# Optimization experiments

Hardware: AMD Instinct MI355X
Metric: run time of the kernel (lower is better)

## Reference

```python
import jax, jax.numpy as jnp
import numpy as np

WINDOW = (2, 8, 8)  # (T, H, W); N = 128
NUM_HEADS = 6
DIM = 192


def _relative_position_index(ws):
    """NxN int index into the relative-position-bias table (faithful port)."""
    d, h, w = np.meshgrid(np.arange(ws[0]), np.arange(ws[1]), np.arange(ws[2]), indexing='ij')
    coords = np.stack([d, h, w]).reshape(3, -1)            # (3, N)
    rel = coords[:, :, None] - coords[:, None, :]          # (3, N, N)
    rel = rel.transpose(1, 2, 0).astype(np.int64)          # (N, N, 3)
    rel[:, :, 0] += ws[0] - 1
    rel[:, :, 1] += ws[1] - 1
    rel[:, :, 2] += ws[2] - 1
    rel[:, :, 0] *= (2 * ws[1] - 1) * (2 * ws[2] - 1)
    rel[:, :, 1] *= 2 * ws[2] - 1
    return rel.sum(-1)                                     # (N, N)


def setup_inputs() -> dict:
    key = jax.random.key(0)
    k1, k2, k3, k4, k5, k6 = jax.random.split(key, 6)
    N = WINDOW[0] * WINDOW[1] * WINDOW[2]                  # 128
    B_ = 1024                                              # num_windows * batch
    nW = 64
    table_len = (2 * WINDOW[0] - 1) * (2 * WINDOW[1] - 1) * (2 * WINDOW[2] - 1)  # 675
    x = jax.random.normal(k1, (B_, N, DIM), dtype=jnp.float32)
    mask = jax.random.normal(k2, (nW, N, N), dtype=jnp.float32)  # additive attn mask
    qkv_w = jax.random.normal(k3, (3 * DIM, DIM), dtype=jnp.float32) * 0.02
    proj_w = jax.random.normal(k4, (DIM, DIM), dtype=jnp.float32) * 0.02
    proj_b = jax.random.normal(k5, (DIM,), dtype=jnp.float32) * 0.02
    rpb_table = jax.random.normal(k6, (table_len, NUM_HEADS), dtype=jnp.float32) * 0.02
    rel_index = jnp.asarray(_relative_position_index(WINDOW), dtype=jnp.int32)
    return {"x": x, "mask": mask, "qkv_w": qkv_w, "proj_w": proj_w,
            "proj_b": proj_b, "rpb_table": rpb_table, "rel_index": rel_index}


def reference(x, mask, qkv_w, proj_w, proj_b, rpb_table, rel_index):
    B_, N, C = x.shape
    H = NUM_HEADS
    hd = C // H
    scale = hd ** (-0.5)
    # qkv projection (no bias, qkv_bias=False)
    qkv = (x @ qkv_w.T).reshape(B_, N, 3, H, hd)
    q, k, v = qkv[:, :, 0], qkv[:, :, 1], qkv[:, :, 2]      # (B_, N, H, hd)
    # windowed attention scores
    attn = jnp.einsum('bnhd,bmhd->bhnm', q * scale, k)      # (B_, H, N, N)
    # gathered relative-position bias: (N, N, H) -> (H, N, N)
    bias = rpb_table[rel_index.reshape(-1)].reshape(N, N, H).transpose(2, 0, 1)
    attn = attn + bias[None]
    # shift-window mask: (nW, N, N) broadcast over batch groups and heads
    nW = mask.shape[0]
    attn = attn.reshape(B_ // nW, nW, H, N, N) + mask[None, :, None]
    attn = attn.reshape(B_, H, N, N)
    attn = jax.nn.softmax(attn, axis=-1)
    out = jnp.einsum('bhnm,bmhd->bnhd', attn, v).reshape(B_, N, C)
    return out @ proj_w.T + proj_b
```

## Files before the change

### kernel.cpp

```cpp
#include <hip/hip_runtime.h>
#include <hip/hip_bf16.h>


typedef float f32x4 __attribute__((ext_vector_type(4)));
typedef short short8 __attribute__((ext_vector_type(8)));
typedef short short4e __attribute__((ext_vector_type(4)));

#define SCALE 0.17677669529663687f
#define LOG2E 1.4426950408889634f
#define QSC (SCALE * LOG2E)

#define GLOAD16(src, dst)                                                      \
  __builtin_amdgcn_global_load_lds(                                            \
      (const __attribute__((address_space(1))) unsigned int*)(const void*)(src),\
      (__attribute__((address_space(3))) unsigned int*)(void*)(dst), 16, 0, 0)

static __device__ __forceinline__ short f2bf(float f) {
  __hip_bfloat16 h = __float2bfloat16(f);
  return __builtin_bit_cast(short, h);
}
static __device__ __forceinline__ f32x4 mfma16(short8 a, short8 b, f32x4 c) {
  return __builtin_amdgcn_mfma_f32_16x16x32_bf16(a, b, c, 0, 0, 0);
}

__global__ __launch_bounds__(256) void prep_w(const float* __restrict__ qkvw,
                                              const float* __restrict__ projw,
                                              short* __restrict__ wbf,
                                              short* __restrict__ pwbf) {
  int t = blockIdx.x * 256 + threadIdx.x;
  const int NQ = 27648;
  float4 f; short* dst;
  if (t < NQ) {
    f = ((const float4*)qkvw)[t];
    int row = (t * 4) / 192, c4 = (t * 4) % 192;
    dst = wbf + row * 192 + (c4 ^ ((row & 7) << 3));
  } else {
    f = ((const float4*)projw)[t - NQ];
    dst = pwbf + (t - NQ) * 4;
  }
  short4e o; o[0] = f2bf(f.x); o[1] = f2bf(f.y); o[2] = f2bf(f.z); o[3] = f2bf(f.w);
  *(short4e*)dst = o;
}

__global__ __launch_bounds__(256) void prep_bm(const int* __restrict__ rel,
                                               const float* __restrict__ table,
                                               const float* __restrict__ mask,
                                               float* __restrict__ bmF) {
  int blk = blockIdx.x;
  int h = blk >> 6, w = blk & 63;
  int tid = threadIdx.x, lane = tid & 63, wave = tid >> 6;
  int lr = lane & 15, r4 = (lane >> 4) * 4;
  const float* mk = mask + (size_t)w * 16384;
  float* dst = bmF + (size_t)blk * 16384;
#pragma unroll
  for (int L = 0; L < 16; ++L) {
    int rf = L >> 3, rg = (L >> 1) & 3, cp = L & 1;
    int row = wave * 32 + rf * 16 + r4 + rg;
    float4 v;
#pragma unroll
    for (int e = 0; e < 4; ++e) {
      int col = (cp * 4 + e) * 16 + lr;
      float bias = table[rel[row * 128 + col] * 6 + h];
      ((float*)&v)[e] = (bias + mk[row * 128 + col]) * LOG2E;
    }
    ((float4*)dst)[L * 256 + tid] = v;
  }
}

__global__ __launch_bounds__(256, 4) void qkv_kernel(const float* __restrict__ x,
                                                     const short* __restrict__ wbf,
                                                     short* __restrict__ qb,
                                                     short* __restrict__ kb,
                                                     short* __restrict__ vb) {
  __shared__ short wt[2][6144];
  char* wtb = (char*)wt;
  const int b = blockIdx.x, tid = threadIdx.x;
  const int wave = tid >> 6, lane = tid & 63;
  const int lr = lane & 15, g = lane >> 4, g8 = g * 8, r4 = g * 4;
  const int rowbase = wave * 32;
  const int xorkey = (lr & 7) << 4;
  const int wl = wave * 1024 + lane * 16;
  const int wu = wave * 1024;

  short8 xa[2][6];
  {
    const float* xr = x + (size_t)b * 24576 + (size_t)(rowbase + lr) * 192;
#pragma unroll
    for (int tf = 0; tf < 2; ++tf)
#pragma unroll
      for (int ks = 0; ks < 6; ++ks) {
        const float* p = xr + tf * 16 * 192 + ks * 32 + g8;
        float4 f0 = *(const float4*)p;
        float4 f1 = *(const float4*)(p + 4);
        short8 v8;
        v8[0] = f2bf(f0.x); v8[1] = f2bf(f0.y); v8[2] = f2bf(f0.z); v8[3] = f2bf(f0.w);
        v8[4] = f2bf(f1.x); v8[5] = f2bf(f1.y); v8[6] = f2bf(f1.z); v8[7] = f2bf(f1.w);
        xa[tf][ks] = v8;
      }
  }
  {
    const char* wsrc = (const char*)wbf;
#pragma unroll
    for (int i = 0; i < 3; ++i)
      GLOAD16(wsrc + i * 4096 + wl, wtb + i * 4096 + wu);
  }
  __syncthreads();

  for (int ch = 0; ch < 12; ++ch) {
    {
      const char* wsrc = (const char*)wbf + (ch + 1) * 12288;
      char* wdst = wtb + ((ch + 1) & 1) * 12288;
#pragma unroll
      for (int i = 0; i < 3; ++i)
        GLOAD16(wsrc + i * 4096 + wl, wdst + i * 4096 + wu);
    }
    const char* wb = wtb + (ch & 1) * 12288;
    f32x4 acc[2][2];
    acc[0][0] = acc[0][1] = acc[1][0] = acc[1][1] = f32x4{0.f, 0.f, 0.f, 0.f};
    __builtin_amdgcn_s_setprio(1);
#pragma unroll
    for (int ks = 0; ks < 6; ++ks) {
      int cx = (ks * 64 + g * 16) ^ xorkey;
      short8 w0 = *(const short8*)(wb + lr * 384 + cx);
      short8 w1 = *(const short8*)(wb + (16 + lr) * 384 + cx);
      acc[0][0] = mfma16(w0, xa[0][ks], acc[0][0]);
      acc[0][1] = mfma16(w0, xa[1][ks], acc[0][1]);
      acc[1][0] = mfma16(w1, xa[0][ks], acc[1][0]);
      acc[1][1] = mfma16(w1, xa[1][ks], acc[1][1]);
    }
    __builtin_amdgcn_s_setprio(0);
    bool isq = (ch < 6);
    short* dst = isq ? qb : kb;
    int h = isq ? ch : ch - 6;
    float sc = isq ? QSC : 1.0f;
    size_t base = ((size_t)b * 6 + h) * 4096;
#pragma unroll
    for (int cf = 0; cf < 2; ++cf)
#pragma unroll
      for (int tf = 0; tf < 2; ++tf) {
        int tok = rowbase + tf * 16 + lr;
        int col = cf * 16 + r4;
        int idx = isq ? col : (col ^ (((tok >> 1) & 3) << 3));
        short4e s4;
        s4[0] = f2bf(acc[cf][tf][0] * sc);
        s4[1] = f2bf(acc[cf][tf][1] * sc);
        s4[2] = f2bf(acc[cf][tf][2] * sc);
        s4[3] = f2bf(acc[cf][tf][3] * sc);
        *(short4e*)&dst[base + (size_t)tok * 32 + idx] = s4;
      }
    __syncthreads();
  }
  for (int ch = 12; ch < 18; ++ch) {
    if (ch < 17) {
      const char* wsrc = (const char*)wbf + (ch + 1) * 12288;
      char* wdst = wtb + ((ch + 1) & 1) * 12288;
#pragma unroll
      for (int i = 0; i < 3; ++i)
        GLOAD16(wsrc + i * 4096 + wl, wdst + i * 4096 + wu);
    }
    const char* wb = wtb + (ch & 1) * 12288;
    f32x4 acc[2][2];
    acc[0][0] = acc[0][1] = acc[1][0] = acc[1][1] = f32x4{0.f, 0.f, 0.f, 0.f};
    __builtin_amdgcn_s_setprio(1);
#pragma unroll
    for (int ks = 0; ks < 6; ++ks) {
      int cx = (ks * 64 + g * 16) ^ xorkey;
      short8 w0 = *(const short8*)(wb + lr * 384 + cx);
      short8 w1 = *(const short8*)(wb + (16 + lr) * 384 + cx);
      acc[0][0] = mfma16(xa[0][ks], w0, acc[0][0]);
      acc[0][1] = mfma16(xa[0][ks], w1, acc[0][1]);
      acc[1][0] = mfma16(xa[1][ks], w0, acc[1][0]);
      acc[1][1] = mfma16(xa[1][ks], w1, acc[1][1]);
    }
    __builtin_amdgcn_s_setprio(0);
    int h = ch - 12;
    size_t base = ((size_t)b * 6 + h) * 4096;
#pragma unroll
    for (int tf = 0; tf < 2; ++tf)
#pragma unroll
      for (int cf = 0; cf < 2; ++cf) {
        int d = cf * 16 + lr;
        int rowpos = rowbase + tf * 16 + r4;
        short4e s4;
        s4[0] = f2bf(acc[tf][cf][0]);
        s4[1] = f2bf(acc[tf][cf][1]);
        s4[2] = f2bf(acc[tf][cf][2]);
        s4[3] = f2bf(acc[tf][cf][3]);
        *(short4e*)&vb[base + (size_t)d * 128 + (rowpos ^ ((d & 15) << 3))] = s4;
      }
    if (ch < 17) __syncthreads();
  }
}

__global__ __launch_bounds__(256, 4) void attn_kernel(const short* __restrict__ qb,
                                                      const short* __restrict__ kb,
                                                      const short* __restrict__ vb,
                                                      const float* __restrict__ bmF,
                                                      char* __restrict__ outc) {
  __shared__ char sbuf[16384];
  __shared__ short p_lds[8192];
  const int bh = blockIdx.x, b = bh / 6, h = bh - b * 6;
  const short* qt = qb + (size_t)bh * 4096;
  const char* kc = (const char*)(kb + (size_t)bh * 4096);
  const char* vc = (const char*)(vb + (size_t)bh * 4096);
  const float4* bm4 = (const float4*)(bmF + ((size_t)h * 64 + (b & 63)) * 16384);
  short* outSlot = (short*)(outc + (size_t)b * 98304 + 49152);
  const int tid = threadIdx.x, wave = tid >> 6, lane = tid & 63;
  const int lr = lane & 15, g = lane >> 4, r4 = g * 4;
  const int rowbase = wave * 32;
  const int wl = wave * 1024 + lane * 16;
  const int wu = wave * 1024;

  GLOAD16(kc + wl,        sbuf + wu);
  GLOAD16(kc + 4096 + wl, sbuf + 4096 + wu);
  GLOAD16(vc + wl,        sbuf + 8192 + wu);
  GLOAD16(vc + 4096 + wl, sbuf + 12288 + wu);
  short8 qaH[2];
  qaH[0] = *(const short8*)&qt[(rowbase + lr) * 32 + g * 8];
  qaH[1] = *(const short8*)&qt[(rowbase + 16 + lr) * 32 + g * 8];
  __syncthreads();

  const char* ksb = sbuf;
  const char* vs = sbuf + 8192;
  char* pw = (char*)p_lds + wave * 4096;
  const int kkey = ((lr >> 1) & 3) << 4;

#pragma unroll
  for (int rf = 0; rf < 2; ++rf) {
    float4 bmv[8];
#pragma unroll
    for (int i = 0; i < 8; ++i) bmv[i] = bm4[(rf * 8 + i) * 256 + tid];
    short8 qa = qaH[rf];
    f32x4 s[8];
    __builtin_amdgcn_s_setprio(1);
#pragma unroll
    for (int cf = 0; cf < 8; ++cf) {
      int krow = cf * 16 + lr;
      short8 kf = *(const short8*)(ksb + krow * 64 + ((g * 16) ^ kkey));
      f32x4 z = {0.f, 0.f, 0.f, 0.f};
      s[cf] = mfma16(qa, kf, z);
    }
    __builtin_amdgcn_s_setprio(0);
    float inv_[4];
#pragma unroll
    for (int rg = 0; rg < 4; ++rg) {
      float4 bb0 = bmv[rg * 2];
      float4 bb1 = bmv[rg * 2 + 1];
      float p0 = exp2f(s[0][rg] + bb0.x);
      float p1 = exp2f(s[1][rg] + bb0.y);
      float p2 = exp2f(s[2][rg] + bb0.z);
      float p3 = exp2f(s[3][rg] + bb0.w);
      float p4 = exp2f(s[4][rg] + bb1.x);
      float p5 = exp2f(s[5][rg] + bb1.y);
      float p6 = exp2f(s[6][rg] + bb1.z);
      float p7 = exp2f(s[7][rg] + bb1.w);
      float sum = ((p0 + p1) + (p2 + p3)) + ((p4 + p5) + (p6 + p7));
#pragma unroll
      for (int o = 1; o < 16; o <<= 1) sum += __shfl_xor(sum, o);
      inv_[rg] = 1.0f / sum;
      int rr = r4 + rg;
      int base = rr * 256 + (lr << 1);
      int swz = rr << 4;
      *(short*)(pw + ((base + 0 * 32) ^ swz)) = f2bf(p0);
      *(short*)(pw + ((base + 1 * 32) ^ swz)) = f2bf(p1);
      *(short*)(pw + ((base + 2 * 32) ^ swz)) = f2bf(p2);
      *(short*)(pw + ((base + 3 * 32) ^ swz)) = f2bf(p3);
      *(short*)(pw + ((base + 4 * 32) ^ swz)) = f2bf(p4);
      *(short*)(pw + ((base + 5 * 32) ^ swz)) = f2bf(p5);
      *(short*)(pw + ((base + 6 * 32) ^ swz)) = f2bf(p6);
      *(short*)(pw + ((base + 7 * 32) ^ swz)) = f2bf(p7);
    }
    f32x4 o0 = {0.f, 0.f, 0.f, 0.f}, o1 = {0.f, 0.f, 0.f, 0.f};
#pragma unroll
    for (int kst = 0; kst < 4; ++kst) {
      short8 pa = *(const short8*)(pw + ((lr * 256 + kst * 64 + g * 16) ^ (lr << 4)));
      short8 vb0 = *(const short8*)(vs + ((lr * 256 + kst * 64 + g * 16) ^ ((lr & 15) << 4)));
      short8 vb1 = *(const short8*)(vs + (((16 + lr) * 256 + kst * 64 + g * 16) ^ (((16 + lr) & 15) << 4)));
      __builtin_amdgcn_s_setprio(1);
      o0 = mfma16(pa, vb0, o0);
      o1 = mfma16(pa, vb1, o1);
      __builtin_amdgcn_s_setprio(0);
    }
#pragma unroll
    for (int rg = 0; rg < 4; ++rg) {
      int tok = rowbase + rf * 16 + r4 + rg;
      float iv = inv_[rg];
      outSlot[(size_t)tok * 192 + h * 32 + lr] = f2bf(o0[rg] * iv);
      outSlot[(size_t)tok * 192 + h * 32 + 16 + lr] = f2bf(o1[rg] * iv);
    }
  }
}

__global__ __launch_bounds__(256, 2) void proj_kernel(const short* __restrict__ pwbf,
                                                      const float* __restrict__ pb,
                                                      float* __restrict__ out) {
  __shared__ short at[24576];
  __shared__ short wt[2][6144];
  const int b = blockIdx.x, tid = threadIdx.x;
  const int wave = tid >> 6, lane = tid & 63;
  const int lr = lane & 15, g = lane >> 4;
  const int g16 = g * 16, r4 = g * 4;
  const int rowbase = wave * 32;
  const int xorkey = (lr & 7) << 4;
  char* atb = (char*)at;
  char* wtb = (char*)wt;

  int wsoff[3], wdoff[3];
#pragma unroll
  for (int i = 0; i < 3; ++i) {
    int idx8 = i * 256 + tid;
    int r = idx8 / 24, c = idx8 - r * 24;
    wsoff[i] = idx8 * 8;
    wdoff[i] = r * 384 + ((c * 16) ^ ((r & 7) << 4));
  }
  short8 wreg[3];
#pragma unroll
  for (int i = 0; i < 3; ++i) wreg[i] = *(const short8*)(pwbf + wsoff[i]);

  const short8* ar = (const short8*)((const char*)out + (size_t)b * 98304 + 49152);
#pragma unroll
  for (int i = 0; i < 12; ++i) {
    int idx8 = i * 256 + tid;
    int r = idx8 / 24, c = idx8 - r * 24;
    short8 v = ar[idx8];
    *(short8*)(atb + r * 384 + ((c * 16) ^ ((r & 7) << 4))) = v;
  }
#pragma unroll
  for (int i = 0; i < 3; ++i) *(short8*)(wtb + wdoff[i]) = wreg[i];
  __syncthreads();

  const int rA0 = (rowbase + lr) * 384, rA1 = rA0 + 16 * 384;
  const int wB0 = lr * 384, wB1 = wB0 + 16 * 384;

  for (int ch = 0; ch < 6; ++ch) {
    if (ch < 5) {
#pragma unroll
      for (int i = 0; i < 3; ++i)
        wreg[i] = *(const short8*)(pwbf + (ch + 1) * 6144 + wsoff[i]);
    }
    const char* wbuf = wtb + (ch & 1) * 12288;
    f32x4 acc[2][2];
    acc[0][0] = acc[0][1] = acc[1][0] = acc[1][1] = f32x4{0.f, 0.f, 0.f, 0.f};
#pragma unroll
    for (int ks = 0; ks < 6; ++ks) {
      int cx = (ks * 64 + g16) ^ xorkey;
      short8 xa0 = *(const short8*)(atb + rA0 + cx);
      short8 xa1 = *(const short8*)(atb + rA1 + cx);
      short8 wf0 = *(const short8*)(wbuf + wB0 + cx);
      short8 wf1 = *(const short8*)(wbuf + wB1 + cx);
      acc[0][0] = mfma16(xa0, wf0, acc[0][0]);
      acc[0][1] = mfma16(xa0, wf1, acc[0][1]);
      acc[1][0] = mfma16(xa1, wf0, acc[1][0]);
      acc[1][1] = mfma16(xa1, wf1, acc[1][1]);
    }
#pragma unroll
    for (int cf = 0; cf < 2; ++cf) {
      int j = ch * 32 + cf * 16 + lr;
      float bj = pb[j];
#pragma unroll
      for (int rf = 0; rf < 2; ++rf)
#pragma unroll
        for (int rg = 0; rg < 4; ++rg) {
          int tok = rowbase + rf * 16 + r4 + rg;
          out[((size_t)b * 128 + tok) * 192 + j] = acc[rf][cf][rg] + bj;
        }
    }
    if (ch < 5) {
#pragma unroll
      for (int i = 0; i < 3; ++i)
        *(short8*)(wtb + ((ch + 1) & 1) * 12288 + wdoff[i]) = wreg[i];
      __syncthreads();
    }
  }
}

extern "C" void kernel_launch(void* const* d_in, const int* in_sizes, int n_in,
                              void* d_out, int out_size, void* d_ws, size_t ws_size,
                              hipStream_t stream) {
  const float* x      = (const float*)d_in[0];
  const float* mask   = (const float*)d_in[1];
  const float* qkv_w  = (const float*)d_in[2];
  const float* proj_w = (const float*)d_in[3];
  const float* proj_b = (const float*)d_in[4];
  const float* table  = (const float*)d_in[5];
  const int*   rel    = (const int*)d_in[6];
  char* ws = (char*)d_ws;
  size_t o = 0;
  float* bmF  = (float*)(ws + o); o += 25165824;
  short* wbf  = (short*)(ws + o); o += 221184;
  short* pwbf = (short*)(ws + o); o += 73728;
  short* qbp  = (short*)(ws + o); o += 50331648;
  short* kbp  = (short*)(ws + o); o += 50331648;
  short* vbp  = (short*)(ws + o); o += 50331648;
  float* out = (float*)d_out;

  prep_w<<<144, 256, 0, stream>>>(qkv_w, proj_w, wbf, pwbf);
  prep_bm<<<384, 256, 0, stream>>>(rel, table, mask, bmF);
  qkv_kernel<<<1024, 256, 0, stream>>>(x, wbf, qbp, kbp, vbp);
  attn_kernel<<<6144, 256, 0, stream>>>(qbp, kbp, vbp, bmF, (char*)d_out);
  proj_kernel<<<1024, 256, 0, stream>>>(pwbf, proj_b, (float*)d_out);
}
```

Measured before the change: 184.2 us.

## Load QKV weights directly from global memory instead of staging through LDS

The QKV projection kernel no longer double-buffers weight chunks in shared memory with async global-to-LDS loads and per-chunk barriers. Each wave now reads its weight fragments straight from global memory (relying on L2/cache reuse) into registers, with the 18-chunk loop fully unrolled and no __syncthreads. The weight prep kernel drops the XOR swizzle to match. Launch bounds shift to 3 blocks/CU for the QKV kernel and 5 for the attention kernel, trading registers for occupancy.

```diff
diff --git a/kernel.cpp b/kernel.cpp
--- a/kernel.cpp
+++ b/kernel.cpp
@@ -30,14 +30,8 @@
   int t = blockIdx.x * 256 + threadIdx.x;
   const int NQ = 27648;
   float4 f; short* dst;
-  if (t < NQ) {
-    f = ((const float4*)qkvw)[t];
-    int row = (t * 4) / 192, c4 = (t * 4) % 192;
-    dst = wbf + row * 192 + (c4 ^ ((row & 7) << 3));
-  } else {
-    f = ((const float4*)projw)[t - NQ];
-    dst = pwbf + (t - NQ) * 4;
-  }
+  if (t < NQ) { f = ((const float4*)qkvw)[t]; dst = wbf + t * 4; }
+  else        { f = ((const float4*)projw)[t - NQ]; dst = pwbf + (t - NQ) * 4; }
   short4e o; o[0] = f2bf(f.x); o[1] = f2bf(f.y); o[2] = f2bf(f.z); o[3] = f2bf(f.w);
   *(short4e*)dst = o;
 }
@@ -67,20 +61,15 @@
   }
 }
 
-__global__ __launch_bounds__(256, 4) void qkv_kernel(const float* __restrict__ x,
+__global__ __launch_bounds__(256, 3) void qkv_kernel(const float* __restrict__ x,
                                                      const short* __restrict__ wbf,
                                                      short* __restrict__ qb,
                                                      short* __restrict__ kb,
                                                      short* __restrict__ vb) {
-  __shared__ short wt[2][6144];
-  char* wtb = (char*)wt;
   const int b = blockIdx.x, tid = threadIdx.x;
   const int wave = tid >> 6, lane = tid & 63;
   const int lr = lane & 15, g = lane >> 4, g8 = g * 8, r4 = g * 4;
   const int rowbase = wave * 32;
-  const int xorkey = (lr & 7) << 4;
-  const int wl = wave * 1024 + lane * 16;
-  const int wu = wave * 1024;
 
   short8 xa[2][6];
   {
@@ -98,101 +87,79 @@
         xa[tf][ks] = v8;
       }
   }
-  {
-    const char* wsrc = (const char*)wbf;
-#pragma unroll
-    for (int i = 0; i < 3; ++i)
-      GLOAD16(wsrc + i * 4096 + wl, wtb + i * 4096 + wu);
-  }
-  __syncthreads();
-
-  for (int ch = 0; ch < 12; ++ch) {
-    {
-      const char* wsrc = (const char*)wbf + (ch + 1) * 12288;
-      char* wdst = wtb + ((ch + 1) & 1) * 12288;
-#pragma unroll
-      for (int i = 0; i < 3; ++i)
-        GLOAD16(wsrc + i * 4096 + wl, wdst + i * 4096 + wu);
-    }
-    const char* wb = wtb + (ch & 1) * 12288;
+
+  const short* w0p = wbf + lr * 192 + g8;
+  const short* w1p = wbf + (16 + lr) * 192 + g8;
+
+#pragma unroll
+  for (int ch = 0; ch < 18; ++ch) {
+    short8 w0[6], w1[6];
+#pragma unroll
+    for (int ks = 0; ks < 6; ++ks) {
+      w0[ks] = *(const short8*)(w0p + ch * 6144 + ks * 32);
+      w1[ks] = *(const short8*)(w1p + ch * 6144 + ks * 32);
+    }
     f32x4 acc[2][2];
     acc[0][0] = acc[0][1] = acc[1][0] = acc[1][1] = f32x4{0.f, 0.f, 0.f, 0.f};
-    __builtin_amdgcn_s_setprio(1);
-#pragma unroll
-    for (int ks = 0; ks < 6; ++ks) {
-      int cx = (ks * 64 + g * 16) ^ xorkey;
-      short8 w0 = *(const short8*)(wb + lr * 384 + cx);
-      short8 w1 = *(const short8*)(wb + (16 + lr) * 384 + cx);
-      acc[0][0] = mfma16(w0, xa[0][ks], acc[0][0]);
-      acc[0][1] = mfma16(w0, xa[1][ks], acc[0][1]);
-      acc[1][0] = mfma16(w1, xa[0][ks], acc[1][0]);
-      acc[1][1] = mfma16(w1, xa[1][ks], acc[1][1]);
-    }
-    __builtin_amdgcn_s_setprio(0);
-    bool isq = (ch < 6);
-    short* dst = isq ? qb : kb;
-    int h = isq ? ch : ch - 6;
-    float sc = isq ? QSC : 1.0f;
-    size_t base = ((size_t)b * 6 + h) * 4096;
-#pragma unroll
-    for (int cf = 0; cf < 2; ++cf)
-#pragma unroll
-      for (int tf = 0; tf < 2; ++tf) {
-        int tok = rowbase + tf * 16 + lr;
-        int col = cf * 16 + r4;
-        int idx = isq ? col : (col ^ (((tok >> 1) & 3) << 3));
-        short4e s4;
-        s4[0] = f2bf(acc[cf][tf][0] * sc);
-        s4[1] = f2bf(acc[cf][tf][1] * sc);
-        s4[2] = f2bf(acc[cf][tf][2] * sc);
-        s4[3] = f2bf(acc[cf][tf][3] * sc);
-        *(short4e*)&dst[base + (size_t)tok * 32 + idx] = s4;
+    if (ch < 12) {
+      __builtin_amdgcn_s_setprio(1);
+#pragma unroll
+      for (int ks = 0; ks < 6; ++ks) {
+        acc[0][0] = mfma16(w0[ks], xa[0][ks], acc[0][0]);
+        acc[0][1] = mfma16(w0[ks], xa[1][ks], acc[0][1]);
+        acc[1][0] = mfma16(w1[ks], xa[0][ks], acc[1][0]);
+        acc[1][1] = mfma16(w1[ks], xa[1][ks], acc[1][1]);
       }
-    __syncthreads();
-  }
-  for (int ch = 12; ch < 18; ++ch) {
-    if (ch < 17) {
-      const char* wsrc = (const char*)wbf + (ch + 1) * 12288;
-      char* wdst = wtb + ((ch + 1) & 1) * 12288;
-#pragma unroll
-      for (int i = 0; i < 3; ++i)
-        GLOAD16(wsrc + i * 4096 + wl, wdst + i * 4096 + wu);
-    }
-    const char* wb = wtb + (ch & 1) * 12288;
-    f32x4 acc[2][2];
-    acc[0][0] = acc[0][1] = acc[1][0] = acc[1][1] = f32x4{0.f, 0.f, 0.f, 0.f};
-    __builtin_amdgcn_s_setprio(1);
-#pragma unroll
-    for (int ks = 0; ks < 6; ++ks) {
-      int cx = (ks * 64 + g * 16) ^ xorkey;
-      short8 w0 = *(const short8*)(wb + lr * 384 + cx);
-      short8 w1 = *(const short8*)(wb + (16 + lr) * 384 + cx);
-      acc[0][0] = mfma16(xa[0][ks], w0, acc[0][0]);
-      acc[0][1] = mfma16(xa[0][ks], w1, acc[0][1]);
-      acc[1][0] = mfma16(xa[1][ks], w0, acc[1][0]);
-      acc[1][1] = mfma16(xa[1][ks], w1, acc[1][1]);
-    }
-    __builtin_amdgcn_s_setprio(0);
-    int h = ch - 12;
-    size_t base = ((size_t)b * 6 + h) * 4096;
-#pragma unroll
-    for (int tf = 0; tf < 2; ++tf)
-#pragma unroll
-      for (int cf = 0; cf < 2; ++cf) {
-        int d = cf * 16 + lr;
-        int rowpos = rowbase + tf * 16 + r4;
-        short4e s4;
-        s4[0] = f2bf(acc[tf][cf][0]);
-        s4[1] = f2bf(acc[tf][cf][1]);
-        s4[2] = f2bf(acc[tf][cf][2]);
-        s4[3] = f2bf(acc[tf][cf][3]);
-        *(short4e*)&vb[base + (size_t)d * 128 + (rowpos ^ ((d & 15) << 3))] = s4;
+      __builtin_amdgcn_s_setprio(0);
+      const bool isq = (ch < 6);
+      short* dst = isq ? qb : kb;
+      const int h = isq ? ch : ch - 6;
+      const float sc = isq ? QSC : 1.0f;
+      size_t base = ((size_t)b * 6 + h) * 4096;
+#pragma unroll
+      for (int cf = 0; cf < 2; ++cf)
+#pragma unroll
+        for (int tf = 0; tf < 2; ++tf) {
+          int tok = rowbase + tf * 16 + lr;
+          int col = cf * 16 + r4;
+          int idx = isq ? col : (col ^ (((tok >> 1) & 3) << 3));
+          short4e s4;
+          s4[0] = f2bf(acc[cf][tf][0] * sc);
+          s4[1] = f2bf(acc[cf][tf][1] * sc);
+          s4[2] = f2bf(acc[cf][tf][2] * sc);
+          s4[3] = f2bf(acc[cf][tf][3] * sc);
+          *(short4e*)&dst[base + (size_t)tok * 32 + idx] = s4;
+        }
+    } else {
+      __builtin_amdgcn_s_setprio(1);
+#pragma unroll
+      for (int ks = 0; ks < 6; ++ks) {
+        acc[0][0] = mfma16(xa[0][ks], w0[ks], acc[0][0]);
+        acc[0][1] = mfma16(xa[0][ks], w1[ks], acc[0][1]);
+        acc[1][0] = mfma16(xa[1][ks], w0[ks], acc[1][0]);
+        acc[1][1] = mfma16(xa[1][ks], w1[ks], acc[1][1]);
       }
-    if (ch < 17) __syncthreads();
-  }
-}
-
-__global__ __launch_bounds__(256, 4) void attn_kernel(const short* __restrict__ qb,
+      __builtin_amdgcn_s_setprio(0);
+      const int h = ch - 12;
+      size_t base = ((size_t)b * 6 + h) * 4096;
+#pragma unroll
+      for (int tf = 0; tf < 2; ++tf)
+#pragma unroll
+        for (int cf = 0; cf < 2; ++cf) {
+          int d = cf * 16 + lr;
+          int rowpos = rowbase + tf * 16 + r4;
+          short4e s4;
+          s4[0] = f2bf(acc[tf][cf][0]);
+          s4[1] = f2bf(acc[tf][cf][1]);
+          s4[2] = f2bf(acc[tf][cf][2]);
+          s4[3] = f2bf(acc[tf][cf][3]);
+          *(short4e*)&vb[base + (size_t)d * 128 + (rowpos ^ ((d & 15) << 3))] = s4;
+        }
+    }
+  }
+}
+
+__global__ __launch_bounds__(256, 5) void attn_kernel(const short* __restrict__ qb,
                                                       const short* __restrict__ kb,
                                                       const short* __restrict__ vb,
                                                       const float* __restrict__ bmF,
```

Measured after the change: 313.9 us. +70.4%, slower.
